# Kernel tuning notes

Measured on AMD Instinct MI355X. Metric: run time of the kernel, lower is better.

Reference implementation:

```python
import jax, jax.numpy as jnp
import numpy as np

N = 40000
E = 640000
D = 128
H = 128
NUM_LAYERS = 3


def _sage_conv(x, src, dst, Wl, Wr, b, num_nodes):
    # message: gather source-node features along each edge  [E, d]
    msg = x[src]
    # mean aggregation into destination nodes
    agg = jax.ops.segment_sum(msg, dst, num_segments=num_nodes)
    deg = jax.ops.segment_sum(jnp.ones((msg.shape[0],), dtype=x.dtype), dst,
                              num_segments=num_nodes)
    agg = agg / jnp.maximum(deg, 1.0)[:, None]
    # out = lin_l(agg) + lin_r(x); pyg lin_l carries the bias, lin_r has none
    return agg @ Wl + b + x @ Wr


def setup_inputs() -> dict:
    key = jax.random.key(0)
    ks = jax.random.split(key, 12)
    x = jax.random.normal(ks[0], (N, D), dtype=jnp.float32)
    edge_index = jax.random.randint(ks[1], (2, E), 0, N, dtype=jnp.int64)
    s = 1.0 / np.sqrt(D)
    inp = {"x": x, "edge_index": edge_index}
    for i in range(NUM_LAYERS):
        inp[f"Wl{i}"] = jax.random.normal(ks[2 + 3 * i], (D, H), dtype=jnp.float32) * s
        inp[f"Wr{i}"] = jax.random.normal(ks[3 + 3 * i], (D, H), dtype=jnp.float32) * s
        inp[f"b{i}"] = jnp.zeros((H,), dtype=jnp.float32)
    return inp


def reference(x, edge_index, Wl0, Wr0, b0, Wl1, Wr1, b1, Wl2, Wr2, b2):
    src, dst = edge_index[0], edge_index[1]
    params = [(Wl0, Wr0, b0), (Wl1, Wr1, b1), (Wl2, Wr2, b2)]
    h = x
    for i, (Wl, Wr, b) in enumerate(params):
        h = _sage_conv(h, src, dst, Wl, Wr, b, N)
        if i != NUM_LAYERS - 1:
            h = jax.nn.relu(h)
            # dropout p=0.5 is identity in eval mode (training=False)
    return h
```

## Files before the change

kernel.cpp:

```cpp
#include <hip/hip_runtime.h>
#include <hip/hip_bf16.h>

#define D 128
#define CAP 64

typedef __attribute__((ext_vector_type(4))) float f32x4;
typedef __attribute__((ext_vector_type(8))) short bf16x8;

static __device__ __forceinline__ unsigned short f2bf(float f) {
    union { float f; unsigned int u; } v; v.f = f;
    unsigned int r = v.u + 0x7fffu + ((v.u >> 16) & 1u);
    return (unsigned short)(r >> 16);
}
static __device__ __forceinline__ float bf2f_lo(unsigned int v) {
    union { unsigned int u; float f; } x; x.u = v << 16; return x.f;
}
static __device__ __forceinline__ float bf2f_hi(unsigned int v) {
    union { unsigned int u; float f; } x; x.u = v & 0xffff0000u; return x.f;
}

__global__ __launch_bounds__(256) void place_cvt_wt_kernel(
    const int* __restrict__ src, const int* __restrict__ dst,
    int* __restrict__ cnt, unsigned short* __restrict__ csr, int E_,
    const float* __restrict__ x, unsigned short* __restrict__ xb, int n4,
    const float* __restrict__ Wl0, const float* __restrict__ Wr0,
    const float* __restrict__ Wl1, const float* __restrict__ Wr1,
    const float* __restrict__ Wl2, const float* __restrict__ Wr2,
    unsigned short* __restrict__ WtB) {
    int bid = blockIdx.x;
    int nplace = (E_ + 255) >> 8;
    if (bid < nplace) {
        int e = bid * 256 + threadIdx.x;
        if (e < E_) {
            int d = dst[e];
            int pos = (d << 6) + atomicAdd(&cnt[d], 1);
            csr[pos] = (unsigned short)src[e];
        }
        return;
    }
    bid -= nplace;
    int ncvt = (n4 + 255) >> 8;
    if (bid < ncvt) {
        int i = bid * 256 + threadIdx.x;
        if (i < n4) {
            float4 v = reinterpret_cast<const float4*>(x)[i];
            ushort4 o;
            o.x = f2bf(v.x); o.y = f2bf(v.y); o.z = f2bf(v.z); o.w = f2bf(v.w);
            reinterpret_cast<ushort4*>(xb)[i] = o;
        }
        return;
    }
    int idx = bid - ncvt;
    int layer = idx >> 4;
    int j = (idx & 15) * 256 + threadIdx.x;
    const float* Wl = (layer == 0) ? Wl0 : (layer == 1) ? Wl1 : Wl2;
    const float* Wr = (layer == 0) ? Wr0 : (layer == 1) ? Wr1 : Wr2;
    unsigned short* Wt = WtB + (size_t)layer * 128 * 256;
    int c = j >> 5;
    int g = j & 31;
    int k0 = g * 8;
    const float* Wsrc = (k0 < 128) ? (Wl + (size_t)k0 * D + c)
                                   : (Wr + (size_t)(k0 - 128) * D + c);
    float v[8];
#pragma unroll
    for (int i = 0; i < 8; ++i) v[i] = Wsrc[(size_t)i * D];
    uint4 o;
    o.x = (unsigned int)f2bf(v[0]) | ((unsigned int)f2bf(v[1]) << 16);
    o.y = (unsigned int)f2bf(v[2]) | ((unsigned int)f2bf(v[3]) << 16);
    o.z = (unsigned int)f2bf(v[4]) | ((unsigned int)f2bf(v[5]) << 16);
    o.w = (unsigned int)f2bf(v[6]) | ((unsigned int)f2bf(v[7]) << 16);
    *reinterpret_cast<uint4*>(Wt + (size_t)c * 256 + k0) = o;
}

__global__ __launch_bounds__(256) void gather_mean_bf16(
    const unsigned short* __restrict__ hb, const int* __restrict__ cnt,
    const unsigned short* __restrict__ csr, unsigned short* __restrict__ aggb,
    int N_) {
    int node = blockIdx.x * 4 + (threadIdx.x >> 6);
    int lane = threadIdx.x & 63;
    if (node >= N_) return;
    int beg = node << 6;
    int dgr = cnt[node];
    int end = beg + dgr;
    int q = lane >> 4;
    int t = lane & 15;

    const uint4* hb4 = reinterpret_cast<const uint4*>(hb);

    float acc[8];
#pragma unroll
    for (int i = 0; i < 8; ++i) acc[i] = 0.f;

#define ACC8(V)                                             \
    acc[0] += bf2f_lo(V.x); acc[1] += bf2f_hi(V.x);         \
    acc[2] += bf2f_lo(V.y); acc[3] += bf2f_hi(V.y);         \
    acc[4] += bf2f_lo(V.z); acc[5] += bf2f_hi(V.z);         \
    acc[6] += bf2f_lo(V.w); acc[7] += bf2f_hi(V.w);

    int e = beg + q;
    for (; e + 12 < end; e += 16) {
        int s0 = csr[e];
        int s1 = csr[e + 4];
        int s2 = csr[e + 8];
        int s3 = csr[e + 12];
        uint4 v0 = hb4[(size_t)s0 * 16 + t];
        uint4 v1 = hb4[(size_t)s1 * 16 + t];
        uint4 v2 = hb4[(size_t)s2 * 16 + t];
        uint4 v3 = hb4[(size_t)s3 * 16 + t];
        ACC8(v0); ACC8(v1); ACC8(v2); ACC8(v3);
    }
    for (; e < end; e += 4) {
        uint4 v0 = hb4[(size_t)csr[e] * 16 + t];
        ACC8(v0);
    }
#undef ACC8

#pragma unroll
    for (int i = 0; i < 8; ++i) {
        acc[i] += __shfl_xor(acc[i], 16, 64);
        acc[i] += __shfl_xor(acc[i], 32, 64);
    }
    if (q == 0) {
        float sc = 1.0f / (float)(dgr > 0 ? dgr : 1);
        uint4 o;
        o.x = (unsigned int)f2bf(acc[0] * sc) | ((unsigned int)f2bf(acc[1] * sc) << 16);
        o.y = (unsigned int)f2bf(acc[2] * sc) | ((unsigned int)f2bf(acc[3] * sc) << 16);
        o.z = (unsigned int)f2bf(acc[4] * sc) | ((unsigned int)f2bf(acc[5] * sc) << 16);
        o.w = (unsigned int)f2bf(acc[6] * sc) | ((unsigned int)f2bf(acc[7] * sc) << 16);
        reinterpret_cast<uint4*>(aggb + (size_t)node * D)[t] = o;
    }
}

template <int MODE>
__global__ __launch_bounds__(1024) void sage_gemm_mfma(
    const unsigned short* __restrict__ hinb, const unsigned short* __restrict__ aggb,
    const unsigned short* __restrict__ WtB, const float* __restrict__ bias,
    void* __restrict__ out, int N_) {
    __shared__ unsigned short sWt[128][264];

    const int tid = threadIdx.x;
    for (int idx = tid; idx < 128 * 32; idx += 1024) {
        int c = idx >> 5, g = idx & 31;
        *reinterpret_cast<uint4*>(&sWt[c][g * 8]) =
            reinterpret_cast<const uint4*>(WtB + (size_t)c * 256)[g];
    }
    __syncthreads();

    const int lane = tid & 63;
    const int w = tid >> 6;
    const int q = lane >> 4;
    const int c = lane & 15;
    const int R = blockIdx.x * 256 + w * 16;

    int r0 = R + c;  if (r0 > N_ - 1) r0 = N_ - 1;

    f32x4 acc[8];
#pragma unroll
    for (int n = 0; n < 8; ++n) acc[n] = (f32x4){0.f, 0.f, 0.f, 0.f};

#pragma unroll
    for (int ks = 0; ks < 8; ++ks) {
        int kg = ks * 32 + q * 8;
        const unsigned short* base = (kg < 128) ? (aggb + kg) : (hinb + (kg - 128));
        bf16x8 a0 = *reinterpret_cast<const bf16x8*>(base + (size_t)r0 * D);
#pragma unroll
        for (int n = 0; n < 8; ++n) {
            bf16x8 b = *reinterpret_cast<const bf16x8*>(&sWt[n * 16 + c][ks * 32 + q * 8]);
            acc[n] = __builtin_amdgcn_mfma_f32_16x16x32_bf16(a0, b, acc[n], 0, 0, 0);
        }
    }

    unsigned short* outb = (unsigned short*)out;
    float* outf = (float*)out;
#pragma unroll
    for (int n = 0; n < 8; ++n) {
        int col = n * 16 + c;
        float bv = bias[col];
#pragma unroll
        for (int r = 0; r < 4; ++r) {
            int row = R + q * 4 + r;
            if (row < N_) {
                float v = acc[n][r] + bv;
                if (MODE == 0) {
                    v = fmaxf(v, 0.f);
                    outb[(size_t)row * D + col] = f2bf(v);
                } else {
                    outf[(size_t)row * D + col] = v;
                }
            }
        }
    }
}

extern "C" void kernel_launch(void* const* d_in, const int* in_sizes, int n_in,
                              void* d_out, int out_size, void* d_ws, size_t ws_size,
                              hipStream_t stream) {
    const float* x = (const float*)d_in[0];
    const int* edge = (const int*)d_in[1];
    const float* Wl[3] = {(const float*)d_in[2], (const float*)d_in[5], (const float*)d_in[8]};
    const float* Wr[3] = {(const float*)d_in[3], (const float*)d_in[6], (const float*)d_in[9]};
    const float* bs[3] = {(const float*)d_in[4], (const float*)d_in[7], (const float*)d_in[10]};

    const int N_ = in_sizes[0] / D;
    const int E_ = in_sizes[1] / 2;
    const int* src = edge;
    const int* dst = edge + E_;

    char* ws = (char*)d_ws;
    size_t bmat = (size_t)N_ * D * sizeof(unsigned short);
    unsigned short* xb = (unsigned short*)ws;
    unsigned short* h1b = (unsigned short*)(ws + bmat);
    unsigned short* aggb = (unsigned short*)(ws + 2 * bmat);
    char* p = ws + 3 * bmat;
    int* cnt = (int*)p;         p += (size_t)N_ * 4;
    unsigned short* WtB = (unsigned short*)p; p += 3 * 128 * 256 * sizeof(unsigned short);
    unsigned short* csr = (unsigned short*)p; p += (size_t)N_ * CAP * 2;

    const int ndeg = (E_ + 255) / 256;
    const int n4 = N_ * D / 4;
    const int ncvt = (n4 + 255) / 256;

    hipMemsetAsync(cnt, 0, (size_t)N_ * sizeof(int), stream);
    place_cvt_wt_kernel<<<ndeg + ncvt + 48, 256, 0, stream>>>(
        src, dst, cnt, csr, E_, x, xb, n4,
        Wl[0], Wr[0], Wl[1], Wr[1], Wl[2], Wr[2], WtB);

    int gemm_blocks = (N_ + 255) / 256;
    int gather_blocks = (N_ + 3) / 4;
    unsigned short* h2b = xb;

    gather_mean_bf16<<<gather_blocks, 256, 0, stream>>>(xb, cnt, csr, aggb, N_);
    sage_gemm_mfma<0><<<gemm_blocks, 1024, 0, stream>>>(xb, aggb, WtB, bs[0], h1b, N_);
    gather_mean_bf16<<<gather_blocks, 256, 0, stream>>>(h1b, cnt, csr, aggb, N_);
    sage_gemm_mfma<0><<<gemm_blocks, 1024, 0, stream>>>(h1b, aggb, WtB + 128 * 256, bs[1], h2b, N_);
    gather_mean_bf16<<<gather_blocks, 256, 0, stream>>>(h2b, cnt, csr, aggb, N_);
    sage_gemm_mfma<1><<<gemm_blocks, 1024, 0, stream>>>(h2b, aggb, WtB + 2 * 128 * 256, bs[2], d_out, N_);
}
```

Measured before the change: 159.5 us.

## Transform features before aggregation and fuse layer-0 GEMM into build kernel

Applies linearity of mean aggregation: each layer first computes z = h·Wl (bf16) and p = h·Wr + b (fp32), then the gather averages z over neighbours and adds p, with ReLU and conversion folded in. Layer 0's GEMM is folded into the CSR-build kernel, which reads fp32 x directly and drops the separate bf16 conversion pass. This lowers the GEMM K dimension per output and lets the gather write the final output. The cost is an extra fp32 pbuf write and read per layer, which adds memory traffic.

Result: slower. 211.1 us (+32.4%).

```diff
diff --git a/kernel.cpp b/kernel.cpp
--- a/kernel.cpp
+++ b/kernel.cpp
@@ -19,18 +19,23 @@
     union { unsigned int u; float f; } x; x.u = v & 0xffff0000u; return x.f;
 }
 
-__global__ __launch_bounds__(256) void place_cvt_wt_kernel(
+__global__ __launch_bounds__(512) void build_kernel(
     const int* __restrict__ src, const int* __restrict__ dst,
     int* __restrict__ cnt, unsigned short* __restrict__ csr, int E_,
-    const float* __restrict__ x, unsigned short* __restrict__ xb, int n4,
+    const float* __restrict__ x,
     const float* __restrict__ Wl0, const float* __restrict__ Wr0,
     const float* __restrict__ Wl1, const float* __restrict__ Wr1,
     const float* __restrict__ Wl2, const float* __restrict__ Wr2,
-    unsigned short* __restrict__ WtB) {
+    const float* __restrict__ b0,
+    unsigned short* __restrict__ WtB,
+    unsigned short* __restrict__ z, float* __restrict__ pbuf, int N_) {
+    __shared__ unsigned short sW[128][136];
+
     int bid = blockIdx.x;
-    int nplace = (E_ + 255) >> 8;
+    const int tid = threadIdx.x;
+    const int nplace = (E_ + 511) >> 9;
     if (bid < nplace) {
-        int e = bid * 256 + threadIdx.x;
+        int e = bid * 512 + tid;
         if (e < E_) {
             int d = dst[e];
             int pos = (d << 6) + atomicAdd(&cnt[d], 1);
@@ -39,43 +44,196 @@
         return;
     }
     bid -= nplace;
-    int ncvt = (n4 + 255) >> 8;
-    if (bid < ncvt) {
-        int i = bid * 256 + threadIdx.x;
-        if (i < n4) {
-            float4 v = reinterpret_cast<const float4*>(x)[i];
-            ushort4 o;
-            o.x = f2bf(v.x); o.y = f2bf(v.y); o.z = f2bf(v.z); o.w = f2bf(v.w);
-            reinterpret_cast<ushort4*>(xb)[i] = o;
-        }
+    if (bid < 16) {
+        int layer = bid >> 3;
+        const float* Wl = layer ? Wl2 : Wl1;
+        const float* Wr = layer ? Wr2 : Wr1;
+        unsigned short* Wt = WtB + (size_t)layer * 256 * 128;
+        int j = (bid & 7) * 512 + tid;
+        int c = j >> 4;
+        int k0 = (j & 15) * 8;
+        const float* Wsrc = (c < 128) ? (Wl + (size_t)k0 * D + c)
+                                      : (Wr + (size_t)k0 * D + (c - 128));
+        float v[8];
+#pragma unroll
+        for (int i = 0; i < 8; ++i) v[i] = Wsrc[(size_t)i * D];
+        uint4 o;
+        o.x = (unsigned int)f2bf(v[0]) | ((unsigned int)f2bf(v[1]) << 16);
+        o.y = (unsigned int)f2bf(v[2]) | ((unsigned int)f2bf(v[3]) << 16);
+        o.z = (unsigned int)f2bf(v[4]) | ((unsigned int)f2bf(v[5]) << 16);
+        o.w = (unsigned int)f2bf(v[6]) | ((unsigned int)f2bf(v[7]) << 16);
+        *reinterpret_cast<uint4*>(Wt + (size_t)c * 128 + k0) = o;
         return;
     }
-    int idx = bid - ncvt;
-    int layer = idx >> 4;
-    int j = (idx & 15) * 256 + threadIdx.x;
-    const float* Wl = (layer == 0) ? Wl0 : (layer == 1) ? Wl1 : Wl2;
-    const float* Wr = (layer == 0) ? Wr0 : (layer == 1) ? Wr1 : Wr2;
-    unsigned short* Wt = WtB + (size_t)layer * 128 * 256;
-    int c = j >> 5;
-    int g = j & 31;
-    int k0 = g * 8;
-    const float* Wsrc = (k0 < 128) ? (Wl + (size_t)k0 * D + c)
-                                   : (Wr + (size_t)(k0 - 128) * D + c);
-    float v[8];
-#pragma unroll
-    for (int i = 0; i < 8; ++i) v[i] = Wsrc[(size_t)i * D];
-    uint4 o;
-    o.x = (unsigned int)f2bf(v[0]) | ((unsigned int)f2bf(v[1]) << 16);
-    o.y = (unsigned int)f2bf(v[2]) | ((unsigned int)f2bf(v[3]) << 16);
-    o.z = (unsigned int)f2bf(v[4]) | ((unsigned int)f2bf(v[5]) << 16);
-    o.w = (unsigned int)f2bf(v[6]) | ((unsigned int)f2bf(v[7]) << 16);
-    *reinterpret_cast<uint4*>(Wt + (size_t)c * 256 + k0) = o;
-}
-
-__global__ __launch_bounds__(256) void gather_mean_bf16(
-    const unsigned short* __restrict__ hb, const int* __restrict__ cnt,
-    const unsigned short* __restrict__ csr, unsigned short* __restrict__ aggb,
-    int N_) {
+    bid -= 16;
+
+    const int lane = tid & 63;
+    const int w = tid >> 6;
+    const int q = lane >> 4;
+    const int c = lane & 15;
+    const int R = bid * 128 + w * 16;
+    int r0 = R + c; if (r0 > N_ - 1) r0 = N_ - 1;
+
+    bf16x8 a[4];
+#pragma unroll
+    for (int ks = 0; ks < 4; ++ks) {
+        const float* ap = x + (size_t)r0 * D + ks * 32 + q * 8;
+        float4 f0 = *reinterpret_cast<const float4*>(ap);
+        float4 f1 = *reinterpret_cast<const float4*>(ap + 4);
+        bf16x8 t;
+        t[0] = (short)f2bf(f0.x); t[1] = (short)f2bf(f0.y);
+        t[2] = (short)f2bf(f0.z); t[3] = (short)f2bf(f0.w);
+        t[4] = (short)f2bf(f1.x); t[5] = (short)f2bf(f1.y);
+        t[6] = (short)f2bf(f1.z); t[7] = (short)f2bf(f1.w);
+        a[ks] = t;
+    }
+
+    for (int idx = tid; idx < 2048; idx += 512) {
+        int cc = idx >> 4, k0 = (idx & 15) * 8;
+        float v[8];
+#pragma unroll
+        for (int i = 0; i < 8; ++i) v[i] = Wl0[(size_t)(k0 + i) * D + cc];
+        uint4 o;
+        o.x = (unsigned int)f2bf(v[0]) | ((unsigned int)f2bf(v[1]) << 16);
+        o.y = (unsigned int)f2bf(v[2]) | ((unsigned int)f2bf(v[3]) << 16);
+        o.z = (unsigned int)f2bf(v[4]) | ((unsigned int)f2bf(v[5]) << 16);
+        o.w = (unsigned int)f2bf(v[6]) | ((unsigned int)f2bf(v[7]) << 16);
+        *reinterpret_cast<uint4*>(&sW[cc][k0]) = o;
+    }
+    __syncthreads();
+    f32x4 acc[8];
+#pragma unroll
+    for (int n = 0; n < 8; ++n) acc[n] = (f32x4){0.f, 0.f, 0.f, 0.f};
+#pragma unroll
+    for (int ks = 0; ks < 4; ++ks)
+#pragma unroll
+        for (int n = 0; n < 8; ++n) {
+            bf16x8 b = *reinterpret_cast<const bf16x8*>(&sW[n * 16 + c][ks * 32 + q * 8]);
+            acc[n] = __builtin_amdgcn_mfma_f32_16x16x32_bf16(a[ks], b, acc[n], 0, 0, 0);
+        }
+#pragma unroll
+    for (int n = 0; n < 8; ++n) {
+        int col = n * 16 + c;
+#pragma unroll
+        for (int r = 0; r < 4; ++r) {
+            int row = R + q * 4 + r;
+            if (row < N_) z[(size_t)row * D + col] = f2bf(acc[n][r]);
+        }
+    }
+    __syncthreads();
+
+    for (int idx = tid; idx < 2048; idx += 512) {
+        int cc = idx >> 4, k0 = (idx & 15) * 8;
+        float v[8];
+#pragma unroll
+        for (int i = 0; i < 8; ++i) v[i] = Wr0[(size_t)(k0 + i) * D + cc];
+        uint4 o;
+        o.x = (unsigned int)f2bf(v[0]) | ((unsigned int)f2bf(v[1]) << 16);
+        o.y = (unsigned int)f2bf(v[2]) | ((unsigned int)f2bf(v[3]) << 16);
+        o.z = (unsigned int)f2bf(v[4]) | ((unsigned int)f2bf(v[5]) << 16);
+        o.w = (unsigned int)f2bf(v[6]) | ((unsigned int)f2bf(v[7]) << 16);
+        *reinterpret_cast<uint4*>(&sW[cc][k0]) = o;
+    }
+    __syncthreads();
+#pragma unroll
+    for (int n = 0; n < 8; ++n) acc[n] = (f32x4){0.f, 0.f, 0.f, 0.f};
+#pragma unroll
+    for (int ks = 0; ks < 4; ++ks)
+#pragma unroll
+        for (int n = 0; n < 8; ++n) {
+            bf16x8 b = *reinterpret_cast<const bf16x8*>(&sW[n * 16 + c][ks * 32 + q * 8]);
+            acc[n] = __builtin_amdgcn_mfma_f32_16x16x32_bf16(a[ks], b, acc[n], 0, 0, 0);
+        }
+#pragma unroll
+    for (int n = 0; n < 8; ++n) {
+        int col = n * 16 + c;
+        float bv = b0[col];
+#pragma unroll
+        for (int r = 0; r < 4; ++r) {
+            int row = R + q * 4 + r;
+            if (row < N_) pbuf[(size_t)row * D + col] = acc[n][r] + bv;
+        }
+    }
+}
+
+__global__ __launch_bounds__(512) void gemm12_kernel(
+    const unsigned short* __restrict__ h, const unsigned short* __restrict__ WtBl,
+    const float* __restrict__ bias, unsigned short* __restrict__ z,
+    float* __restrict__ pbuf, int N_) {
+    __shared__ unsigned short sW[128][136];
+
+    const int tid = threadIdx.x;
+    const int lane = tid & 63;
+    const int w = tid >> 6;
+    const int q = lane >> 4;
+    const int c = lane & 15;
+    const int R = blockIdx.x * 128 + w * 16;
+    int r0 = R + c; if (r0 > N_ - 1) r0 = N_ - 1;
+
+    bf16x8 a[4];
+#pragma unroll
+    for (int ks = 0; ks < 4; ++ks)
+        a[ks] = *reinterpret_cast<const bf16x8*>(h + (size_t)r0 * D + ks * 32 + q * 8);
+
+    for (int idx = tid; idx < 2048; idx += 512) {
+        int cc = idx >> 4, g = idx & 15;
+        *reinterpret_cast<uint4*>(&sW[cc][g * 8]) =
+            reinterpret_cast<const uint4*>(WtBl + (size_t)cc * 128)[g];
+    }
+    __syncthreads();
+    f32x4 acc[8];
+#pragma unroll
+    for (int n = 0; n < 8; ++n) acc[n] = (f32x4){0.f, 0.f, 0.f, 0.f};
+#pragma unroll
+    for (int ks = 0; ks < 4; ++ks)
+#pragma unroll
+        for (int n = 0; n < 8; ++n) {
+            bf16x8 b = *reinterpret_cast<const bf16x8*>(&sW[n * 16 + c][ks * 32 + q * 8]);
+            acc[n] = __builtin_amdgcn_mfma_f32_16x16x32_bf16(a[ks], b, acc[n], 0, 0, 0);
+        }
+#pragma unroll
+    for (int n = 0; n < 8; ++n) {
+        int col = n * 16 + c;
+#pragma unroll
+        for (int r = 0; r < 4; ++r) {
+            int row = R + q * 4 + r;
+            if (row < N_) z[(size_t)row * D + col] = f2bf(acc[n][r]);
+        }
+    }
+    __syncthreads();
+
+    for (int idx = tid; idx < 2048; idx += 512) {
+        int cc = idx >> 4, g = idx & 15;
+        *reinterpret_cast<uint4*>(&sW[cc][g * 8]) =
+            reinterpret_cast<const uint4*>(WtBl + (size_t)(128 + cc) * 128)[g];
+    }
+    __syncthreads();
+#pragma unroll
+    for (int n = 0; n < 8; ++n) acc[n] = (f32x4){0.f, 0.f, 0.f, 0.f};
+#pragma unroll
+    for (int ks = 0; ks < 4; ++ks)
+#pragma unroll
+        for (int n = 0; n < 8; ++n) {
+            bf16x8 b = *reinterpret_cast<const bf16x8*>(&sW[n * 16 + c][ks * 32 + q * 8]);
+            acc[n] = __builtin_amdgcn_mfma_f32_16x16x32_bf16(a[ks], b, acc[n], 0, 0, 0);
+        }
+#pragma unroll
+    for (int n = 0; n < 8; ++n) {
+        int col = n * 16 + c;
+        float bv = bias[col];
+#pragma unroll
+        for (int r = 0; r < 4; ++r) {
+            int row = R + q * 4 + r;
+            if (row < N_) pbuf[(size_t)row * D + col] = acc[n][r] + bv;
+        }
+    }
+}
+
+template <int MODE>
+__global__ __launch_bounds__(256) void gather_finish(
+    const unsigned short* __restrict__ z, const int* __restrict__ cnt,
+    const unsigned short* __restrict__ csr, const float* __restrict__ pbuf,
+    void* __restrict__ out, int N_) {
     int node = blockIdx.x * 4 + (threadIdx.x >> 6);
     int lane = threadIdx.x & 63;
     if (node >= N_) return;
@@ -85,7 +243,7 @@
     int q = lane >> 4;
     int t = lane & 15;
 
-    const uint4* hb4 = reinterpret_cast<const uint4*>(hb);
+    const uint4* hb4 = reinterpret_cast<const uint4*>(z);
 
     float acc[8];
 #pragma unroll
@@ -122,72 +280,27 @@
     }
     if (q == 0) {
         float sc = 1.0f / (float)(dgr > 0 ? dgr : 1);
-        uint4 o;
-        o.x = (unsigned int)f2bf(acc[0] * sc) | ((unsigned int)f2bf(acc[1] * sc) << 16);
-        o.y = (unsigned int)f2bf(acc[2] * sc) | ((unsigned int)f2bf(acc[3] * sc) << 16);
-        o.z = (unsigned int)f2bf(acc[4] * sc) | ((unsigned int)f2bf(acc[5] * sc) << 16);
-        o.w = (unsigned int)f2bf(acc[6] * sc) | ((unsigned int)f2bf(acc[7] * sc) << 16);
-        reinterpret_cast<uint4*>(aggb + (size_t)node * D)[t] = o;
-    }
-}
-
-template <int MODE>
-__global__ __launch_bounds__(1024) void sage_gemm_mfma(
-    const unsigned short* __restrict__ hinb, const unsigned short* __restrict__ aggb,
-    const unsigned short* __restrict__ WtB, const float* __restrict__ bias,
-    void* __restrict__ out, int N_) {
-    __shared__ unsigned short sWt[128][264];
-
-    const int tid = threadIdx.x;
-    for (int idx = tid; idx < 128 * 32; idx += 1024) {
-        int c = idx >> 5, g = idx & 31;
-        *reinterpret_cast<uint4*>(&sWt[c][g * 8]) =
-            reinterpret_cast<const uint4*>(WtB + (size_t)c * 256)[g];
-    }
-    __syncthreads();
-
-    const int lane = tid & 63;
-    const int w = tid >> 6;
-    const int q = lane >> 4;
-    const int c = lane & 15;
-    const int R = blockIdx.x * 256 + w * 16;
-
-    int r0 = R + c;  if (r0 > N_ - 1) r0 = N_ - 1;
-
-    f32x4 acc[8];
-#pragma unroll
-    for (int n = 0; n < 8; ++n) acc[n] = (f32x4){0.f, 0.f, 0.f, 0.f};
-
-#pragma unroll
-    for (int ks = 0; ks < 8; ++ks) {
-        int kg = ks * 32 + q * 8;
-        const unsigned short* base = (kg < 128) ? (aggb + kg) : (hinb + (kg - 128));
-        bf16x8 a0 = *reinterpret_cast<const bf16x8*>(base + (size_t)r0 * D);
-#pragma unroll
-        for (int n = 0; n < 8; ++n) {
-            bf16x8 b = *reinterpret_cast<const bf16x8*>(&sWt[n * 16 + c][ks * 32 + q * 8]);
-            acc[n] = __builtin_amdgcn_mfma_f32_16x16x32_bf16(a0, b, acc[n], 0, 0, 0);
-        }
-    }
-
-    unsigned short* outb = (unsigned short*)out;
-    float* outf = (float*)out;
-#pragma unroll
-    for (int n = 0; n < 8; ++n) {
-        int col = n * 16 + c;
-        float bv = bias[col];
-#pragma unroll
-        for (int r = 0; r < 4; ++r) {
-            int row = R + q * 4 + r;
-            if (row < N_) {
-                float v = acc[n][r] + bv;
-                if (MODE == 0) {
-                    v = fmaxf(v, 0.f);
-                    outb[(size_t)row * D + col] = f2bf(v);
-                } else {
-                    outf[(size_t)row * D + col] = v;
-                }
-            }
+        const float* pr = pbuf + (size_t)node * D + t * 8;
+        float4 p0 = *reinterpret_cast<const float4*>(pr);
+        float4 p1 = *reinterpret_cast<const float4*>(pr + 4);
+        float v[8];
+        v[0] = acc[0] * sc + p0.x; v[1] = acc[1] * sc + p0.y;
+        v[2] = acc[2] * sc + p0.z; v[3] = acc[3] * sc + p0.w;
+        v[4] = acc[4] * sc + p1.x; v[5] = acc[5] * sc + p1.y;
+        v[6] = acc[6] * sc + p1.z; v[7] = acc[7] * sc + p1.w;
+        if (MODE == 0) {
+#pragma unroll
+            for (int i = 0; i < 8; ++i) v[i] = fmaxf(v[i], 0.f);
+            uint4 o;
+            o.x = (unsigned int)f2bf(v[0]) | ((unsigned int)f2bf(v[1]) << 16);
+            o.y = (unsigned int)f2bf(v[2]) | ((unsigned int)f2bf(v[3]) << 16);
+            o.z = (unsigned int)f2bf(v[4]) | ((unsigned int)f2bf(v[5]) << 16);
+            o.w = (unsigned int)f2bf(v[6]) | ((unsigned int)f2bf(v[7]) << 16);
+            reinterpret_cast<uint4*>((unsigned short*)out + (size_t)node * D)[t] = o;
+        } else {
+            float* of = (float*)out + (size_t)node * D + t * 8;
+            *reinterpret_cast<float4*>(of) = (float4){v[0], v[1], v[2], v[3]};
+            *reinterpret_cast<float4*>(of + 4) = (float4){v[4], v[5], v[6], v[7]};
         }
     }
 }
@@ -197,9 +310,15 @@
                               hipStream_t stream) {
     const float* x = (const float*)d_in[0];
     const int* edge = (const int*)d_in[1];
-    const float* Wl[3] = {(const float*)d_in[2], (const float*)d_in[5], (const float*)d_in[8]};
-    const float* Wr[3] = {(const float*)d_in[3], (const float*)d_in[6], (const float*)d_in[9]};
-    const float* bs[3] = {(const float*)d_in[4], (const float*)d_in[7], (const float*)d_in[10]};
+    const float* Wl0 = (const float*)d_in[2];
+    const float* Wr0 = (const float*)d_in[3];
+    const float* b0 = (const float*)d_in[4];
+    const float* Wl1 = (const float*)d_in[5];
+    const float* Wr1 = (const float*)d_in[6];
+    const float* b1 = (const float*)d_in[7];
+    const float* Wl2 = (const float*)d_in[8];
+    const float* Wr2 = (const float*)d_in[9];
+    const float* b2 = (const float*)d_in[10];
 
     const int N_ = in_sizes[0] / D;
     const int E_ = in_sizes[1] / 2;
@@ -208,31 +327,26 @@
 
     char* ws = (char*)d_ws;
     size_t bmat = (size_t)N_ * D * sizeof(unsigned short);
-    unsigned short* xb = (unsigned short*)ws;
-    unsigned short* h1b = (unsigned short*)(ws + bmat);
-    unsigned short* aggb = (unsigned short*)(ws + 2 * bmat);
-    char* p = ws + 3 * bmat;
+    unsigned short* z = (unsigned short*)ws;
+    unsigned short* h = (unsigned short*)(ws + bmat);
+    float* pbuf = (float*)(ws + 2 * bmat);
+    char* p = ws + 2 * bmat + (size_t)N_ * D * sizeof(float);
     int* cnt = (int*)p;         p += (size_t)N_ * 4;
-    unsigned short* WtB = (unsigned short*)p; p += 3 * 128 * 256 * sizeof(unsigned short);
+    unsigned short* WtB = (unsigned short*)p; p += 2 * 256 * 128 * sizeof(unsigned short);
     unsigned short* csr = (unsigned short*)p; p += (size_t)N_ * CAP * 2;
 
-    const int ndeg = (E_ + 255) / 256;
-    const int n4 = N_ * D / 4;
-    const int ncvt = (n4 + 255) / 256;
+    const int nplace = (E_ + 511) / 512;
+    const int gemmB = (N_ + 127) / 128;
+    const int gatherB = (N_ + 3) / 4;
 
     hipMemsetAsync(cnt, 0, (size_t)N_ * sizeof(int), stream);
-    place_cvt_wt_kernel<<<ndeg + ncvt + 48, 256, 0, stream>>>(
-        src, dst, cnt, csr, E_, x, xb, n4,
-        Wl[0], Wr[0], Wl[1], Wr[1], Wl[2], Wr[2], WtB);
-
-    int gemm_blocks = (N_ + 255) / 256;
-    int gather_blocks = (N_ + 3) / 4;
-    unsigned short* h2b = xb;
-
-    gather_mean_bf16<<<gather_blocks, 256, 0, stream>>>(xb, cnt, csr, aggb, N_);
-    sage_gemm_mfma<0><<<gemm_blocks, 1024, 0, stream>>>(xb, aggb, WtB, bs[0], h1b, N_);
-    gather_mean_bf16<<<gather_blocks, 256, 0, stream>>>(h1b, cnt, csr, aggb, N_);
-    sage_gemm_mfma<0><<<gemm_blocks, 1024, 0, stream>>>(h1b, aggb, WtB + 128 * 256, bs[1], h2b, N_);
-    gather_mean_bf16<<<gather_blocks, 256, 0, stream>>>(h2b, cnt, csr, aggb, N_);
-    sage_gemm_mfma<1><<<gemm_blocks, 1024, 0, stream>>>(h2b, aggb, WtB + 2 * 128 * 256, bs[2], d_out, N_);
-}
+    build_kernel<<<nplace + 16 + gemmB, 512, 0, stream>>>(
+        src, dst, cnt, csr, E_, x, Wl0, Wr0, Wl1, Wr1, Wl2, Wr2, b0,
+        WtB, z, pbuf, N_);
+
+    gather_finish<0><<<gatherB, 256, 0, stream>>>(z, cnt, csr, pbuf, h, N_);
+    gemm12_kernel<<<gemmB, 512, 0, stream>>>(h, WtB, b1, z, pbuf, N_);
+    gather_finish<0><<<gatherB, 256, 0, stream>>>(z, cnt, csr, pbuf, h, N_);
+    gemm12_kernel<<<gemmB, 512, 0, stream>>>(h, WtB + 256 * 128, b2, z, pbuf, N_);
+    gather_finish<1><<<gatherB, 256, 0, stream>>>(z, cnt, csr, pbuf, d_out, N_);
+}
```
